# Kernel optimization log

Measured on AMD Instinct MI355X. Metric: run time of the kernel, lower is better.

## Reference

```python
import jax, jax.numpy as jnp
import numpy as np

N_NODES = 100000
N_EDGES = 1600000
IN_F, H_F, OUT_F = 128, 64, 32


def setup_inputs() -> dict:
    key = jax.random.key(0)
    k = jax.random.split(key, 8)
    x = jax.random.normal(k[0], (N_NODES, IN_F), dtype=jnp.float32)
    edge_index = jax.random.randint(k[1], (2, N_EDGES), 0, N_NODES, dtype=jnp.int32).astype(jnp.int64)
    edge_weight = jax.random.uniform(k[2], (N_EDGES,), dtype=jnp.float32)
    # GCNConv params (Glorot-ish scale)
    W1 = jax.random.normal(k[3], (IN_F, H_F), dtype=jnp.float32) / np.sqrt(IN_F)
    b1 = jnp.zeros((H_F,), dtype=jnp.float32)
    W2 = jax.random.normal(k[4], (H_F, OUT_F), dtype=jnp.float32) / np.sqrt(H_F)
    b2 = jnp.zeros((OUT_F,), dtype=jnp.float32)
    return {"x": x, "edge_index": edge_index, "edge_weight": edge_weight,
            "W1": W1, "b1": b1, "W2": W2, "b2": b2}


def _gcn_norm(edge_index, edge_weight, num_nodes):
    """PyG gcn_norm: add self-loops (weight 1), symmetric D^-1/2 A D^-1/2."""
    row, col = edge_index[0], edge_index[1]
    loop = jnp.arange(num_nodes, dtype=row.dtype)
    row = jnp.concatenate([row, loop])
    col = jnp.concatenate([col, loop])
    ew = jnp.concatenate([edge_weight, jnp.ones((num_nodes,), edge_weight.dtype)])
    deg = jax.ops.segment_sum(ew, col, num_segments=num_nodes)
    dinv = jnp.where(deg > 0, jax.lax.rsqrt(deg), jnp.zeros_like(deg))
    norm = dinv[row] * ew * dinv[col]
    return row, col, norm


def _gcn_conv(x, row, col, norm, W, b):
    h = x @ W                                   # dense projection [N, F_out]
    msg = norm[:, None] * h[row]                # gather + scale   [E+N, F_out]
    agg = jax.ops.segment_sum(msg, col, num_segments=x.shape[0])  # scatter-add
    return agg + b


def reference(x, edge_index, edge_weight, W1, b1, W2, b2):
    # dropout(p=0.6) is identity in eval mode
    row, col, norm = _gcn_norm(edge_index, edge_weight, x.shape[0])
    h = jax.nn.relu(_gcn_conv(x, row, col, norm, W1, b1))
    out = _gcn_conv(h, row, col, norm, W2, b2)
    return out
```

## Files before the change

kernel.cpp:

```cpp
#include <hip/hip_runtime.h>
#include <cstdint>
#include <cstddef>


#define IN_F 128
#define H_F 64
#define OUT_F 32

#define DEG_SCALE 16777216.0f
#define DEG_MASK ((1ULL << 40) - 1)

__global__ void k_detect_idx64(const long long* __restrict__ idx, int n_nodes,
                               int* __restrict__ flag) {
    __shared__ int ok;
    if (threadIdx.x == 0) ok = 1;
    __syncthreads();
    long long v = idx[threadIdx.x];
    if (v < 0 || v >= (long long)n_nodes) atomicAnd(&ok, 0);
    __syncthreads();
    if (threadIdx.x == 0) *flag = ok;
}

__device__ __forceinline__ void decode_edge(const long long* __restrict__ idx64, int E,
                                            int e, int flag, int& r, int& c) {
    if (flag) {
        r = (int)idx64[e];
        c = (int)idx64[E + e];
    } else {
        const int* p = (const int*)idx64;
        r = p[e];
        c = p[E + e];
    }
}

__global__ void k_edge_prep(const long long* __restrict__ idx64, const float* __restrict__ ew,
                            const int* __restrict__ flag,
                            unsigned long long* __restrict__ deg_cnt, int E) {
    int e = blockIdx.x * 256 + threadIdx.x;
    if (e >= E) return;
    int r, c;
    decode_edge(idx64, E, e, *flag, r, c);
    unsigned long long w = (unsigned long long)(ew[e] * DEG_SCALE + 0.5f);
    atomicAdd(&deg_cnt[c], (1ULL << 40) | w);
}

__global__ void k_unpack(const unsigned long long* __restrict__ deg_cnt,
                         int* __restrict__ cnt, float* __restrict__ dinv, int n) {
    int i = blockIdx.x * blockDim.x + threadIdx.x;
    if (i < n) {
        unsigned long long p = deg_cnt[i];
        cnt[i] = (int)(p >> 40);
        float deg = (float)(p & DEG_MASK) * (1.0f / DEG_SCALE);
        dinv[i] = rsqrtf(deg + 1.0f);
    }
}

__global__ void k_scan_partial(const int* __restrict__ cnt, int* __restrict__ partial, int n) {
    __shared__ int s[256];
    int i = blockIdx.x * 256 + threadIdx.x;
    s[threadIdx.x] = (i < n) ? cnt[i] : 0;
    __syncthreads();
    for (int st = 128; st > 0; st >>= 1) {
        if (threadIdx.x < st) s[threadIdx.x] += s[threadIdx.x + st];
        __syncthreads();
    }
    if (threadIdx.x == 0) partial[blockIdx.x] = s[0];
}

__global__ void k_scan_top(int* __restrict__ partial, int nparts) {
    __shared__ int s[512];
    int t = threadIdx.x;
    int mine = (t < nparts) ? partial[t] : 0;
    s[t] = mine;
    __syncthreads();
    for (int st = 1; st < 512; st <<= 1) {
        int v = (t >= st) ? s[t - st] : 0;
        __syncthreads();
        s[t] += v;
        __syncthreads();
    }
    if (t < nparts) partial[t] = s[t] - mine;
}

__global__ void k_scan_final(const int* __restrict__ cnt, const int* __restrict__ partial,
                             int* __restrict__ off, int* __restrict__ cursor, int n) {
    __shared__ int s[256];
    int t = threadIdx.x;
    int i = blockIdx.x * 256 + t;
    int mine = (i < n) ? cnt[i] : 0;
    s[t] = mine;
    __syncthreads();
    for (int st = 1; st < 256; st <<= 1) {
        int v = (t >= st) ? s[t - st] : 0;
        __syncthreads();
        s[t] += v;
        __syncthreads();
    }
    if (i < n) {
        int ex = s[t] - mine + partial[blockIdx.x];
        off[i] = ex;
        cursor[i] = ex;
    }
}

__global__ void k_reorder(const long long* __restrict__ idx64, const float* __restrict__ ew,
                          const int* __restrict__ flag, const float* __restrict__ dinv,
                          int* __restrict__ cursor, int2* __restrict__ csr, int E) {
    int e = blockIdx.x * 256 + threadIdx.x;
    if (e >= E) return;
    int r, c;
    decode_edge(idx64, E, e, *flag, r, c);
    float v = dinv[r] * ew[e] * dinv[c];
    int pos = atomicAdd(&cursor[c], 1);
    csr[pos] = make_int2(r, __float_as_int(v));
}

template <int K, int F>
__global__ void k_gemm(const float* __restrict__ X, const float* __restrict__ W,
                       float* __restrict__ Y, int N) {
    __shared__ float Ws[K * F];
    for (int t = threadIdx.x; t < (K * F) / 4; t += blockDim.x) {
        reinterpret_cast<float4*>(Ws)[t] = reinterpret_cast<const float4*>(W)[t];
    }
    __syncthreads();
    constexpr int NPI = 256 / F;
    constexpr int ITERS = 64 / NPI;
    const int f = threadIdx.x % F;
    const int nl = threadIdx.x / F;
    const int base = blockIdx.x * 64;
    for (int it = 0; it < ITERS; ++it) {
        int n = base + it * NPI + nl;
        if (n < N) {
            const float4* x4 = reinterpret_cast<const float4*>(X + (size_t)n * K);
            float acc = 0.f;
#pragma unroll
            for (int k4 = 0; k4 < K / 4; ++k4) {
                float4 xv = x4[k4];
                acc += xv.x * Ws[(4 * k4 + 0) * F + f];
                acc += xv.y * Ws[(4 * k4 + 1) * F + f];
                acc += xv.z * Ws[(4 * k4 + 2) * F + f];
                acc += xv.w * Ws[(4 * k4 + 3) * F + f];
            }
            Y[(size_t)n * F + f] = acc;
        }
    }
}

template <int F, bool RELU>
__global__ void k_agg(const float* __restrict__ Yin, const int* __restrict__ off,
                      const int* __restrict__ cnt, const int2* __restrict__ csr,
                      const float* __restrict__ dinv, const float* __restrict__ bias,
                      float* __restrict__ Out, int N) {
    const int lane = threadIdx.x % F;
    const int sub = threadIdx.x / F;
    const int n = blockIdx.x * (256 / F) + sub;
    if (n >= N) return;
    float d = dinv[n];
    float acc = d * d * Yin[(size_t)n * F + lane];
    int j = off[n];
    const int e = j + cnt[n];
    for (; j + 1 < e; j += 2) {
        int2 c0 = csr[j], c1 = csr[j + 1];
        acc += __int_as_float(c0.y) * Yin[(size_t)c0.x * F + lane];
        acc += __int_as_float(c1.y) * Yin[(size_t)c1.x * F + lane];
    }
    if (j < e) {
        int2 c0 = csr[j];
        acc += __int_as_float(c0.y) * Yin[(size_t)c0.x * F + lane];
    }
    acc += bias[lane];
    if (RELU) acc = acc > 0.f ? acc : 0.f;
    Out[(size_t)n * F + lane] = acc;
}

extern "C" void kernel_launch(void* const* d_in, const int* in_sizes, int n_in,
                              void* d_out, int out_size, void* d_ws, size_t ws_size,
                              hipStream_t stream) {
    const float* x = (const float*)d_in[0];
    const long long* idx = (const long long*)d_in[1];
    const float* ew = (const float*)d_in[2];
    const float* W1 = (const float*)d_in[3];
    const float* b1 = (const float*)d_in[4];
    const float* W2 = (const float*)d_in[5];
    const float* b2 = (const float*)d_in[6];
    float* out = (float*)d_out;

    const int N = in_sizes[0] / IN_F;
    const int E = in_sizes[2];
    const int nparts = (N + 255) / 256;

    char* ws = (char*)d_ws;
    size_t off_b = 0;
    auto alloc = [&](size_t bytes) {
        void* p = ws + off_b;
        off_b += (bytes + 255) & ~(size_t)255;
        return p;
    };
    unsigned long long* deg_cnt = (unsigned long long*)alloc((size_t)N * 8);
    int* cnt = (int*)alloc((size_t)N * 4);
    float* dinv = (float*)alloc((size_t)N * 4);
    int* offs = (int*)alloc((size_t)N * 4);
    int* cursor = (int*)alloc((size_t)N * 4);
    int* partial = (int*)alloc((size_t)nparts * 4);
    int* flag = (int*)alloc(256);
    int2* csr = (int2*)alloc((size_t)E * 8);
    float* XW1 = (float*)alloc((size_t)N * H_F * 4);
    float* H = (float*)alloc((size_t)N * H_F * 4);
    float* HW2 = (float*)alloc((size_t)N * OUT_F * 4);

    k_detect_idx64<<<1, 64, 0, stream>>>(idx, N, flag);
    hipMemsetAsync(deg_cnt, 0, (size_t)N * 8, stream);
    k_edge_prep<<<(E + 255) / 256, 256, 0, stream>>>(idx, ew, flag, deg_cnt, E);
    k_unpack<<<(N + 255) / 256, 256, 0, stream>>>(deg_cnt, cnt, dinv, N);
    k_scan_partial<<<nparts, 256, 0, stream>>>(cnt, partial, N);
    k_scan_top<<<1, 512, 0, stream>>>(partial, nparts);
    k_scan_final<<<nparts, 256, 0, stream>>>(cnt, partial, offs, cursor, N);
    k_reorder<<<(E + 255) / 256, 256, 0, stream>>>(idx, ew, flag, dinv, cursor, csr, E);

    k_gemm<IN_F, H_F><<<(N + 63) / 64, 256, 0, stream>>>(x, W1, XW1, N);
    k_agg<H_F, true><<<(N + 3) / 4, 256, 0, stream>>>(XW1, offs, cnt, csr, dinv, b1, H, N);

    k_gemm<H_F, OUT_F><<<(N + 63) / 64, 256, 0, stream>>>(H, W2, HW2, N);
    k_agg<OUT_F, false><<<(N + 7) / 8, 256, 0, stream>>>(HW2, offs, cnt, csr, dinv, b2, out, N);
}
```

Measured before the change: 558.9 us.

## Register-tile the dense GEMM kernels with shared-memory X staging

Rewrites the node-feature projection GEMM so each block stages a 128-row chunk of X, transposed, into shared memory in K-chunks of 32. Each thread then computes a RPT×4 register tile of outputs with float4 LDS reads and float4 stores. This replaces the old one-output-per-thread scheme, which reread X rows from global memory per output column and did scalar LDS reads of W. The cost is more registers and shared memory per block, which may lower occupancy. The GEMMs are only part of a pipeline dominated by CSR build and gather aggregation.

```diff
diff --git a/kernel.cpp b/kernel.cpp
--- a/kernel.cpp
+++ b/kernel.cpp
@@ -116,32 +116,72 @@
 }
 
 template <int K, int F>
-__global__ void k_gemm(const float* __restrict__ X, const float* __restrict__ W,
-                       float* __restrict__ Y, int N) {
+__global__ __launch_bounds__(256) void k_gemm(const float* __restrict__ X,
+                                              const float* __restrict__ W,
+                                              float* __restrict__ Y, int N) {
+    constexpr int KC = 32;
+    constexpr int TC = F / 4;
+    constexpr int TR = 256 / TC;
+    constexpr int RPT = 128 / TR;
+    constexpr int XP = 132;
+    __shared__ float Xs[KC][XP];
     __shared__ float Ws[K * F];
-    for (int t = threadIdx.x; t < (K * F) / 4; t += blockDim.x) {
+
+    for (int t = threadIdx.x; t < (K * F) / 4; t += 256)
         reinterpret_cast<float4*>(Ws)[t] = reinterpret_cast<const float4*>(W)[t];
-    }
-    __syncthreads();
-    constexpr int NPI = 256 / F;
-    constexpr int ITERS = 64 / NPI;
-    const int f = threadIdx.x % F;
-    const int nl = threadIdx.x / F;
-    const int base = blockIdx.x * 64;
-    for (int it = 0; it < ITERS; ++it) {
-        int n = base + it * NPI + nl;
+
+    const int tc = threadIdx.x % TC;
+    const int tr = threadIdx.x / TC;
+    const int row0 = blockIdx.x * 128;
+
+    float acc[RPT][4];
+#pragma unroll
+    for (int i = 0; i < RPT; ++i)
+#pragma unroll
+        for (int j = 0; j < 4; ++j) acc[i][j] = 0.f;
+
+    for (int kc = 0; kc < K; kc += KC) {
+        __syncthreads();
+#pragma unroll
+        for (int t = threadIdx.x; t < 128 * (KC / 4); t += 256) {
+            int r = t / (KC / 4);
+            int k4 = t % (KC / 4);
+            int n = row0 + r;
+            float4 v = (n < N) ? *reinterpret_cast<const float4*>(X + (size_t)n * K + kc + k4 * 4)
+                               : make_float4(0.f, 0.f, 0.f, 0.f);
+            Xs[k4 * 4 + 0][r] = v.x;
+            Xs[k4 * 4 + 1][r] = v.y;
+            Xs[k4 * 4 + 2][r] = v.z;
+            Xs[k4 * 4 + 3][r] = v.w;
+        }
+        __syncthreads();
+#pragma unroll
+        for (int k = 0; k < KC; ++k) {
+            float4 w = *reinterpret_cast<const float4*>(&Ws[(kc + k) * F + tc * 4]);
+            float xr[RPT];
+#pragma unroll
+            for (int i = 0; i < RPT / 4; ++i) {
+                float4 xv = *reinterpret_cast<const float4*>(&Xs[k][tr * RPT + i * 4]);
+                xr[i * 4 + 0] = xv.x;
+                xr[i * 4 + 1] = xv.y;
+                xr[i * 4 + 2] = xv.z;
+                xr[i * 4 + 3] = xv.w;
+            }
+#pragma unroll
+            for (int i = 0; i < RPT; ++i) {
+                acc[i][0] += xr[i] * w.x;
+                acc[i][1] += xr[i] * w.y;
+                acc[i][2] += xr[i] * w.z;
+                acc[i][3] += xr[i] * w.w;
+            }
+        }
+    }
+#pragma unroll
+    for (int i = 0; i < RPT; ++i) {
+        int n = row0 + tr * RPT + i;
         if (n < N) {
-            const float4* x4 = reinterpret_cast<const float4*>(X + (size_t)n * K);
-            float acc = 0.f;
-#pragma unroll
-            for (int k4 = 0; k4 < K / 4; ++k4) {
-                float4 xv = x4[k4];
-                acc += xv.x * Ws[(4 * k4 + 0) * F + f];
-                acc += xv.y * Ws[(4 * k4 + 1) * F + f];
-                acc += xv.z * Ws[(4 * k4 + 2) * F + f];
-                acc += xv.w * Ws[(4 * k4 + 3) * F + f];
-            }
-            Y[(size_t)n * F + f] = acc;
+            float4 v = make_float4(acc[i][0], acc[i][1], acc[i][2], acc[i][3]);
+            *reinterpret_cast<float4*>(Y + (size_t)n * F + tc * 4) = v;
         }
     }
 }
@@ -217,9 +257,9 @@
     k_scan_final<<<nparts, 256, 0, stream>>>(cnt, partial, offs, cursor, N);
     k_reorder<<<(E + 255) / 256, 256, 0, stream>>>(idx, ew, flag, dinv, cursor, csr, E);
 
-    k_gemm<IN_F, H_F><<<(N + 63) / 64, 256, 0, stream>>>(x, W1, XW1, N);
+    k_gemm<IN_F, H_F><<<(N + 127) / 128, 256, 0, stream>>>(x, W1, XW1, N);
     k_agg<H_F, true><<<(N + 3) / 4, 256, 0, stream>>>(XW1, offs, cnt, csr, dinv, b1, H, N);
 
-    k_gemm<H_F, OUT_F><<<(N + 63) / 64, 256, 0, stream>>>(H, W2, HW2, N);
+    k_gemm<H_F, OUT_F><<<(N + 127) / 128, 256, 0, stream>>>(H, W2, HW2, N);
     k_agg<OUT_F, false><<<(N + 7) / 8, 256, 0, stream>>>(HW2, offs, cnt, csr, dinv, b2, out, N);
 }
```

Result: faster. 516.5 us (-7.6%).
